# Kernel optimization log

Measured on AMD Instinct MI355X. Metric: run time of the kernel, lower is better.

Reference implementation:

```python
import jax, jax.numpy as jnp
import numpy as np
import math

B, S, D = 2, 1024, 1024
H = 16
HD = D // H
E = 8
DFF = 4096
EPS = 1e-5


def _ln(x, g, b):
    m = jnp.mean(x, axis=-1, keepdims=True)
    v = jnp.mean((x - m) ** 2, axis=-1, keepdims=True)
    return (x - m) / jnp.sqrt(v + EPS) * g + b


def setup_inputs() -> dict:
    key = jax.random.key(0)
    ks = jax.random.split(key, 16)
    s = 0.02
    inp = {
        'src': jax.random.normal(ks[0], (B, S, D), jnp.float32),
        'qw': jax.random.normal(ks[1], (D, D), jnp.float32) * s,
        'kw': jax.random.normal(ks[2], (D, D), jnp.float32) * s,
        'vw': jax.random.normal(ks[3], (D, D), jnp.float32) * s,
        'ow': jax.random.normal(ks[4], (D, D), jnp.float32) * s,
        'gate_w': jax.random.normal(ks[5], (D, D), jnp.float32) * s,
        'gate_b': jax.random.normal(ks[6], (D,), jnp.float32) * s,
        'scale_w': jax.random.normal(ks[7], (H, HD), jnp.float32) * s,
        'n1_g': jnp.ones((D,), jnp.float32),
        'n1_b': jnp.zeros((D,), jnp.float32),
        'n2_g': jnp.ones((D,), jnp.float32),
        'n2_b': jnp.zeros((D,), jnp.float32),
        'moe_gate_w': jax.random.normal(ks[8], (D, E), jnp.float32) * s,
        'moe_gate_b': jnp.zeros((E,), jnp.float32),
        'w1': jax.random.normal(ks[9], (E, D, DFF), jnp.float32) * s,
        'b1': jnp.zeros((E, DFF), jnp.float32),
        'ln_g': jnp.ones((E, DFF), jnp.float32),
        'ln_b': jnp.zeros((E, DFF), jnp.float32),
        'w2': jax.random.normal(ks[10], (E, DFF, D), jnp.float32) * s,
        'b2': jnp.zeros((E, D), jnp.float32),
        'res_scale': jnp.ones((E,), jnp.float32),
    }
    return inp


def _forward(src, qw, kw, vw, ow, gate_w, gate_b, scale_w, n1_g, n1_b, n2_g, n2_b,
             moe_gate_w, moe_gate_b, w1, b1, ln_g, ln_b, w2, b2, res_scale):
    # ---- MemoAttention (non-flash path, eval: no dropout, no mask) ----
    q = (src @ qw).reshape(B, S, H, HD).transpose(0, 2, 1, 3)  # [B,H,S,HD]
    k = (src @ kw).reshape(B, S, H, HD).transpose(0, 2, 1, 3)
    v = (src @ vw).reshape(B, S, H, HD).transpose(0, 2, 1, 3)
    scores = jnp.einsum('bhqd,bhkd->bhqk', q, k) / math.sqrt(HD)
    # dynamic per-(head,query) scale gate
    scale = jax.nn.sigmoid(jnp.einsum('bhsd,hd->bhs', q, scale_w)) * 2.0
    scores = scores * scale[..., None]
    attn = jax.nn.softmax(scores, axis=-1)
    out = jnp.einsum('bhqk,bhkd->bhqd', attn, v)
    out = out.transpose(0, 2, 1, 3).reshape(B, S, D)
    gate = jax.nn.sigmoid(out @ gate_w + gate_b)
    attn_out = (out * gate) @ ow

    x = _ln(src + attn_out, n1_g, n1_b)

    # ---- MoE FFN (top-2 routing; eval: no gate noise; capacity never exceeded) ----
    xf = x.reshape(-1, D)                      # [T, D]
    T = xf.shape[0]
    logits = xf @ moe_gate_w + moe_gate_b      # [T, E]
    top_v, top_i = jax.lax.top_k(logits, 2)
    # NB: original sums BOTH top-k softmax weights per token (== 1.0), and the
    wsum = jnp.sum(jax.nn.softmax(top_v, axis=-1), axis=-1)   # [T] (== 1)
    e_sel = jnp.max(top_i, axis=-1)                           # [T]
    # dense per-expert FFN on all tokens, then per-token select (masked compute)
    h = jnp.einsum('td,edf->etf', xf, w1) + b1[:, None, :]    # [E,T,DFF]
    h = _ln(h, ln_g[:, None, :], ln_b[:, None, :])
    h = jax.nn.gelu(h, approximate=False)                     # torch nn.GELU (erf)
    y = jnp.einsum('etf,efd->etd', h, w2) + b2[:, None, :]    # [E,T,D]
    y = y * res_scale[:, None, None] + xf[None]
    sel = jnp.take_along_axis(y, e_sel[None, :, None], axis=0)[0]  # [T,D]
    moe_out = (sel * wsum[:, None]).reshape(B, S, D)

    return _ln(x + moe_out, n2_g, n2_b)


def reference(src, qw, kw, vw, ow, gate_w, gate_b, scale_w, n1_g, n1_b, n2_g, n2_b,
              moe_gate_w, moe_gate_b, w1, b1, ln_g, ln_b, w2, b2, res_scale):
    return _forward(src, qw, kw, vw, ow, gate_w, gate_b, scale_w, n1_g, n1_b,
                    n2_g, n2_b, moe_gate_w, moe_gate_b, w1, b1, ln_g, ln_b,
                    w2, b2, res_scale)
```

## Files before the change

### kernel.cpp

```cpp
#include <hip/hip_runtime.h>
#include <math.h>

#define TOK    2048
#define DMODEL 1024
#define NHEAD  16
#define HDIM   64
#define NEXP   8
#define DFFN   4096

typedef unsigned short u16;
typedef __attribute__((ext_vector_type(8))) short short8;
typedef __attribute__((ext_vector_type(4))) float floatx4;

__device__ __forceinline__ float sigmoidf_(float x) { return 1.f / (1.f + expf(-x)); }

__device__ __forceinline__ u16 f2bf(float f) {
  union { float f; unsigned u; } v; v.f = f;
  unsigned r = v.u + 0x7FFFu + ((v.u >> 16) & 1u);
  return (u16)(r >> 16);
}
__device__ __forceinline__ float bf2f(u16 h) {
  union { unsigned u; float f; } v; v.u = ((unsigned)h) << 16; return v.f;
}

__device__ __forceinline__ void gload16(const void* g, void* l) {
  __builtin_amdgcn_global_load_lds((const __attribute__((address_space(1))) void*)g,
                                   (__attribute__((address_space(3))) void*)l, 16, 0, 0);
}

__device__ __forceinline__ float blockReduceSum256(float val) {
  __shared__ float ws_[4];
  #pragma unroll
  for (int off = 32; off; off >>= 1) val += __shfl_down(val, off);
  int lane = threadIdx.x & 63, w = threadIdx.x >> 6;
  if (lane == 0) ws_[w] = val;
  __syncthreads();
  float r = ws_[0] + ws_[1] + ws_[2] + ws_[3];
  __syncthreads();
  return r;
}

__global__ __launch_bounds__(256) void split_kernel(
    const float* __restrict__ X, u16* __restrict__ Hi, u16* __restrict__ Lo) {
  const int i = blockIdx.x * 256 + threadIdx.x;
  const float4 v = ((const float4*)X)[i];
  const float f[4] = {v.x, v.y, v.z, v.w};
  union { u16 s[4]; uint2 u; } h, l;
  #pragma unroll
  for (int j = 0; j < 4; ++j) {
    h.s[j] = f2bf(f[j]);
    l.s[j] = f2bf(f[j] - bf2f(h.s[j]));
  }
  ((uint2*)Hi)[i] = h.u;
  ((uint2*)Lo)[i] = l.u;
}

template<bool LO>
__global__ __launch_bounds__(256) void wt_conv_kernel(
    const float* __restrict__ W, u16* __restrict__ Whi, u16* __restrict__ Wlo,
    int K, int N) {
  const size_t z = blockIdx.z;
  W   += z * (size_t)K * N;
  Whi += z * (size_t)K * N;
  if (LO) Wlo += z * (size_t)K * N;
  __shared__ float tile[32][33];
  const int n0 = blockIdx.x * 32, k0 = blockIdx.y * 32;
  const int r = threadIdx.x >> 3, c4 = (threadIdx.x & 7) * 4;
  const float4 v = *(const float4*)&W[(size_t)(k0 + r) * N + n0 + c4];
  tile[r][c4+0] = v.x; tile[r][c4+1] = v.y; tile[r][c4+2] = v.z; tile[r][c4+3] = v.w;
  __syncthreads();
  union { u16 s[4]; uint2 u; } h, l;
  #pragma unroll
  for (int j = 0; j < 4; ++j) {
    const float f = tile[c4 + j][r];
    h.s[j] = f2bf(f);
    if (LO) l.s[j] = f2bf(f - bf2f(h.s[j]));
  }
  *(uint2*)&Whi[(size_t)(n0 + r) * K + k0 + c4] = h.u;
  if (LO) *(uint2*)&Wlo[(size_t)(n0 + r) * K + k0 + c4] = l.u;
}

template<int EPI>
__global__ __launch_bounds__(256, 3) void gemm_split_kernel(
    const u16* __restrict__ Ahi, const u16* __restrict__ Alo,
    const u16* __restrict__ Whi, const u16* __restrict__ Wlo,
    const float* __restrict__ bias, const float* __restrict__ mul,
    float* __restrict__ Cf, u16* __restrict__ Chi, u16* __restrict__ Clo,
    int M, int N, int K) {
  __shared__ u16 Ah[128*64], Al[128*64], Bh[64*64], Bl[64*64];
  const int tid = threadIdx.x;
  const int lane = tid & 63, wave = tid >> 6;
  const int row0 = blockIdx.y * 128, col0 = blockIdx.x * 64;
  const int wm = (wave & 1) * 64, wn = (wave >> 1) * 32;
  const int mr = tid >> 3;
  const int ksrc = (tid & 7) ^ ((tid >> 3) & 7);
  const floatx4 zero = {0.f, 0.f, 0.f, 0.f};
  floatx4 acc[4][2];
  #pragma unroll
  for (int i = 0; i < 4; ++i)
    #pragma unroll
    for (int j = 0; j < 2; ++j) acc[i][j] = zero;

  for (int k0 = 0; k0 < K; k0 += 64) {
    __syncthreads();
    #pragma unroll
    for (int p = 0; p < 4; ++p) {
      const size_t ga = (size_t)(row0 + p * 32 + mr) * K + (k0 + ksrc * 8);
      const size_t off = (size_t)(p * 256 + wave * 64) * 16;
      gload16(Ahi + ga, (char*)Ah + off);
      gload16(Alo + ga, (char*)Al + off);
    }
    #pragma unroll
    for (int p = 0; p < 2; ++p) {
      const size_t gb = (size_t)(col0 + p * 32 + mr) * K + (k0 + ksrc * 8);
      const size_t off = (size_t)(p * 256 + wave * 64) * 16;
      gload16(Whi + gb, (char*)Bh + off);
      gload16(Wlo + gb, (char*)Bl + off);
    }
    __syncthreads();
    #pragma unroll
    for (int kk = 0; kk < 2; ++kk) {
      short8 ah[4], al[4], bh[2], bl[2];
      #pragma unroll
      for (int i = 0; i < 4; ++i) {
        const int ml = wm + i * 16 + (lane & 15);
        const int cm = (kk * 4 + (lane >> 4)) ^ (ml & 7);
        ah[i] = *(const short8*)&Ah[ml * 64 + cm * 8];
        al[i] = *(const short8*)&Al[ml * 64 + cm * 8];
      }
      #pragma unroll
      for (int j = 0; j < 2; ++j) {
        const int nl = wn + j * 16 + (lane & 15);
        const int cn = (kk * 4 + (lane >> 4)) ^ (nl & 7);
        bh[j] = *(const short8*)&Bh[nl * 64 + cn * 8];
        bl[j] = *(const short8*)&Bl[nl * 64 + cn * 8];
      }
      #pragma unroll
      for (int i = 0; i < 4; ++i)
        #pragma unroll
        for (int j = 0; j < 2; ++j) {
          acc[i][j] = __builtin_amdgcn_mfma_f32_16x16x32_bf16(ah[i], bh[j], acc[i][j], 0, 0, 0);
          acc[i][j] = __builtin_amdgcn_mfma_f32_16x16x32_bf16(al[i], bh[j], acc[i][j], 0, 0, 0);
          acc[i][j] = __builtin_amdgcn_mfma_f32_16x16x32_bf16(ah[i], bl[j], acc[i][j], 0, 0, 0);
        }
    }
  }
  const int cl = lane & 15, quad = lane >> 4;
  #pragma unroll
  for (int i = 0; i < 4; ++i)
    #pragma unroll
    for (int j = 0; j < 2; ++j) {
      const int col = col0 + wn + j * 16 + cl;
      #pragma unroll
      for (int r = 0; r < 4; ++r) {
        const int row = row0 + wm + i * 16 + quad * 4 + r;
        const float v = acc[i][j][r];
        if (EPI == 0) {
          Cf[(size_t)row * N + col] = v;
        } else if (EPI == 1) {
          const float s = sigmoidf_(v + bias[col]);
          const float g = s * mul[(size_t)row * N + col];
          const u16 hh = f2bf(g);
          Chi[(size_t)row * N + col] = hh;
          Clo[(size_t)row * N + col] = f2bf(g - bf2f(hh));
        } else {
          const u16 hh = f2bf(v);
          Chi[(size_t)row * N + col] = hh;
          Clo[(size_t)row * N + col] = f2bf(v - bf2f(hh));
        }
      }
    }
}

template<int EPI>
__global__ __launch_bounds__(256, 4) void gemm_moe_kernel(
    const u16* __restrict__ A, const u16* __restrict__ Wt,
    const float* __restrict__ bias,
    const int* __restrict__ perm, const int* __restrict__ offs,
    const int* __restrict__ counts,
    u16* __restrict__ Hout, float* __restrict__ P0, float* __restrict__ P1,
    int N, int K, int e_base) {
  const int z = blockIdx.z;
  const int ez = (EPI == 0) ? z : (z & 3);
  const int ks = (EPI == 0) ? 0 : (z >> 2);
  const int e = e_base + ez;
  const int ne = counts[e];
  const int tm = blockIdx.y;
  if (tm * 128 >= ne) return;
  const int kbeg = (EPI == 0) ? 0 : ks * (K >> 1);
  const int kend = (EPI == 0) ? K : kbeg + (K >> 1);
  __shared__ u16 As_[128*64], Bs_[64*64];
  __shared__ int toks[128];
  const int tid = threadIdx.x;
  if (tid < 128) {
    const int idx = tm * 128 + tid;
    toks[tid] = perm[offs[e] + (idx < ne ? idx : 0)];
  }
  __syncthreads();
  const int lane = tid & 63, wave = tid >> 6;
  const int wm = (wave & 1) * 64, wn = (wave >> 1) * 32;
  const int mr = tid >> 3;
  const int ksrc = (tid & 7) ^ ((tid >> 3) & 7);
  size_t abase[4];
  #pragma unroll
  for (int p = 0; p < 4; ++p) abase[p] = (size_t)toks[p * 32 + mr] * K;
  const u16* We = Wt + (size_t)ez * N * K;
  const int col0 = blockIdx.x * 64;
  const floatx4 zero = {0.f, 0.f, 0.f, 0.f};
  floatx4 acc[4][2];
  #pragma unroll
  for (int i = 0; i < 4; ++i)
    #pragma unroll
    for (int j = 0; j < 2; ++j) acc[i][j] = zero;

  for (int k0 = kbeg; k0 < kend; k0 += 64) {
    __syncthreads();
    #pragma unroll
    for (int p = 0; p < 4; ++p) {
      const size_t off = (size_t)(p * 256 + wave * 64) * 16;
      gload16(A + abase[p] + (k0 + ksrc * 8), (char*)As_ + off);
    }
    #pragma unroll
    for (int p = 0; p < 2; ++p) {
      const size_t off = (size_t)(p * 256 + wave * 64) * 16;
      gload16(We + (size_t)(col0 + p * 32 + mr) * K + (k0 + ksrc * 8), (char*)Bs_ + off);
    }
    __syncthreads();
    #pragma unroll
    for (int kk = 0; kk < 2; ++kk) {
      short8 a[4], b[2];
      #pragma unroll
      for (int i = 0; i < 4; ++i) {
        const int ml = wm + i * 16 + (lane & 15);
        const int cm = (kk * 4 + (lane >> 4)) ^ (ml & 7);
        a[i] = *(const short8*)&As_[ml * 64 + cm * 8];
      }
      #pragma unroll
      for (int j = 0; j < 2; ++j) {
        const int nl = wn + j * 16 + (lane & 15);
        const int cn = (kk * 4 + (lane >> 4)) ^ (nl & 7);
        b[j] = *(const short8*)&Bs_[nl * 64 + cn * 8];
      }
      #pragma unroll
      for (int i = 0; i < 4; ++i)
        #pragma unroll
        for (int j = 0; j < 2; ++j)
          acc[i][j] = __builtin_amdgcn_mfma_f32_16x16x32_bf16(a[i], b[j], acc[i][j], 0, 0, 0);
    }
  }
  const int cl = lane & 15, quad = lane >> 4;
  float* Pp = (EPI == 1) ? (ks ? P1 : P0) : nullptr;
  #pragma unroll
  for (int i = 0; i < 4; ++i)
    #pragma unroll
    for (int j = 0; j < 2; ++j) {
      const int col = col0 + wn + j * 16 + cl;
      #pragma unroll
      for (int r = 0; r < 4; ++r) {
        const int rl = wm + i * 16 + quad * 4 + r;
        if (tm * 128 + rl < ne) {
          const int tok = toks[rl];
          if (EPI == 0)
            Hout[(size_t)tok * N + col] = f2bf(acc[i][j][r] + bias[(size_t)e * N + col]);
          else
            Pp[(size_t)tok * N + col] = acc[i][j][r];
        }
      }
    }
}

__global__ __launch_bounds__(256) void vt_trans_kernel(
    const u16* __restrict__ QKh, const u16* __restrict__ QKl,
    u16* __restrict__ Vth, u16* __restrict__ Vtl) {
  const int tt = blockIdx.x;
  const int bh = blockIdx.y;
  const int b = bh >> 4, h = bh & 15;
  __shared__ u16 th[64][72], tl[64][72];
  const int t = threadIdx.x;
  const int r = t >> 3, c8 = (t & 7) * 8;
  #pragma unroll
  for (int p = 0; p < 2; ++p) {
    const int tok = p * 32 + r;
    const size_t g = ((size_t)b * 1024 + tt * 64 + tok) * 3072 + 2048 + h * 64 + c8;
    *(uint4*)&th[tok][c8] = *(const uint4*)&QKh[g];
    *(uint4*)&tl[tok][c8] = *(const uint4*)&QKl[g];
  }
  __syncthreads();
  #pragma unroll
  for (int p = 0; p < 2; ++p) {
    const int d = p * 32 + r;
    union { u16 s[8]; uint4 u; } oh, ol;
    #pragma unroll
    for (int j = 0; j < 8; ++j) { oh.s[j] = th[c8 + j][d]; ol.s[j] = tl[c8 + j][d]; }
    const size_t g = ((size_t)bh * 64 + d) * 1024 + tt * 64 + c8;
    *(uint4*)&Vth[g] = oh.u;
    *(uint4*)&Vtl[g] = ol.u;
  }
}

__global__ __launch_bounds__(256, 2) void attn_mfma_kernel(
    const u16* __restrict__ QKh, const u16* __restrict__ QKl,
    const u16* __restrict__ Vth, const u16* __restrict__ Vtl,
    const float* __restrict__ scale_w,
    float* __restrict__ AOf, u16* __restrict__ AOh, u16* __restrict__ AOl) {
  const int qt = blockIdx.x, h = blockIdx.y, b = blockIdx.z;
  __shared__ u16 Kh[64*64], Kl[64*64], Vh[64*64], Vl[64*64];
  __shared__ u16 Ph[4][16*72], Pl[4][16*72];
  const int tid = threadIdx.x, lane = tid & 63, wave = tid >> 6;
  const int i15 = lane & 15, quad = lane >> 4;
  const floatx4 zero = {0.f, 0.f, 0.f, 0.f};

  short8 qh[2], ql[2];
  const size_t qrow = ((size_t)b * 1024 + qt * 64 + wave * 16 + i15) * 3072 + h * 64;
  #pragma unroll
  for (int kk = 0; kk < 2; ++kk) {
    qh[kk] = *(const short8*)&QKh[qrow + kk * 32 + quad * 8];
    ql[kk] = *(const short8*)&QKl[qrow + kk * 32 + quad * 8];
  }
  float dot = 0.f;
  #pragma unroll
  for (int kk = 0; kk < 2; ++kk)
    #pragma unroll
    for (int j = 0; j < 8; ++j) {
      const float sw = scale_w[h * 64 + kk * 32 + quad * 8 + j];
      dot += (bf2f((u16)qh[kk][j]) + bf2f((u16)ql[kk][j])) * sw;
    }
  dot += __shfl_xor(dot, 16);
  dot += __shfl_xor(dot, 32);
  const float g = 2.f * sigmoidf_(dot) * 0.125f;
  float stot[4];
  #pragma unroll
  for (int r = 0; r < 4; ++r) stot[r] = __shfl(g, (lane >> 4) * 4 + r);

  float m_r[4], l_r[4];
  floatx4 Of[4];
  #pragma unroll
  for (int r = 0; r < 4; ++r) { m_r[r] = -1e30f; l_r[r] = 0.f; }
  #pragma unroll
  for (int f = 0; f < 4; ++f) Of[f] = zero;
  u16* PhW = Ph[wave];
  u16* PlW = Pl[wave];

  const int sr = tid >> 3, sc = ((tid & 7) ^ ((tid >> 3) & 7)) * 8;
  for (int kt = 0; kt < 16; ++kt) {
    __syncthreads();
    #pragma unroll
    for (int p = 0; p < 2; ++p) {
      const int row = p * 32 + sr;
      const size_t off = (size_t)(p * 256 + wave * 64) * 16;
      const size_t kg = ((size_t)b * 1024 + kt * 64 + row) * 3072 + 1024 + h * 64 + sc;
      gload16(QKh + kg, (char*)Kh + off);
      gload16(QKl + kg, (char*)Kl + off);
      const size_t vg = ((size_t)(b * 16 + h) * 64 + row) * 1024 + kt * 64 + sc;
      gload16(Vth + vg, (char*)Vh + off);
      gload16(Vtl + vg, (char*)Vl + off);
    }
    __syncthreads();
    float pm[4][4];
    #pragma unroll
    for (int jn = 0; jn < 4; ++jn) {
      floatx4 a = zero;
      #pragma unroll
      for (int kk = 0; kk < 2; ++kk) {
        const int n = jn * 16 + i15;
        const int ch = ((kk * 4 + quad) ^ (n & 7)) * 8;
        const short8 bh = *(const short8*)&Kh[n * 64 + ch];
        const short8 bl = *(const short8*)&Kl[n * 64 + ch];
        a = __builtin_amdgcn_mfma_f32_16x16x32_bf16(qh[kk], bh, a, 0, 0, 0);
        a = __builtin_amdgcn_mfma_f32_16x16x32_bf16(ql[kk], bh, a, 0, 0, 0);
        a = __builtin_amdgcn_mfma_f32_16x16x32_bf16(qh[kk], bl, a, 0, 0, 0);
      }
      #pragma unroll
      for (int r = 0; r < 4; ++r) pm[jn][r] = a[r] * stot[r];
    }
    float alpha[4];
    #pragma unroll
    for (int r = 0; r < 4; ++r) {
      float mx = fmaxf(fmaxf(pm[0][r], pm[1][r]), fmaxf(pm[2][r], pm[3][r]));
      mx = fmaxf(mx, __shfl_xor(mx, 1));
      mx = fmaxf(mx, __shfl_xor(mx, 2));
      mx = fmaxf(mx, __shfl_xor(mx, 4));
      mx = fmaxf(mx, __shfl_xor(mx, 8));
      const float mn = fmaxf(m_r[r], mx);
      alpha[r] = expf(m_r[r] - mn);
      m_r[r] = mn;
      float rs = 0.f;
      #pragma unroll
      for (int jn = 0; jn < 4; ++jn) { pm[jn][r] = expf(pm[jn][r] - mn); rs += pm[jn][r]; }
      rs += __shfl_xor(rs, 1);
      rs += __shfl_xor(rs, 2);
      rs += __shfl_xor(rs, 4);
      rs += __shfl_xor(rs, 8);
      l_r[r] = l_r[r] * alpha[r] + rs;
    }
    #pragma unroll
    for (int f = 0; f < 4; ++f)
      #pragma unroll
      for (int r = 0; r < 4; ++r) Of[f][r] *= alpha[r];
    #pragma unroll
    for (int jn = 0; jn < 4; ++jn)
      #pragma unroll
      for (int r = 0; r < 4; ++r) {
        const int a = (quad * 4 + r) * 72 + jn * 16 + i15;
        const u16 hh = f2bf(pm[jn][r]);
        PhW[a] = hh;
        PlW[a] = f2bf(pm[jn][r] - bf2f(hh));
      }
    #pragma unroll
    for (int kk = 0; kk < 2; ++kk) {
      const short8 pah = *(const short8*)&PhW[i15 * 72 + kk * 32 + quad * 8];
      const short8 pal = *(const short8*)&PlW[i15 * 72 + kk * 32 + quad * 8];
      #pragma unroll
      for (int f = 0; f < 4; ++f) {
        const int d = f * 16 + i15;
        const int ch = ((kk * 4 + quad) ^ (d & 7)) * 8;
        const short8 vbh = *(const short8*)&Vh[d * 64 + ch];
        const short8 vbl = *(const short8*)&Vl[d * 64 + ch];
        Of[f] = __builtin_amdgcn_mfma_f32_16x16x32_bf16(pah, vbh, Of[f], 0, 0, 0);
        Of[f] = __builtin_amdgcn_mfma_f32_16x16x32_bf16(pal, vbh, Of[f], 0, 0, 0);
        Of[f] = __builtin_amdgcn_mfma_f32_16x16x32_bf16(pah, vbl, Of[f], 0, 0, 0);
      }
    }
  }
  float inv[4];
  #pragma unroll
  for (int r = 0; r < 4; ++r) inv[r] = 1.f / l_r[r];
  #pragma unroll
  for (int f = 0; f < 4; ++f)
    #pragma unroll
    for (int r = 0; r < 4; ++r) {
      const size_t row = (size_t)b * 1024 + qt * 64 + wave * 16 + quad * 4 + r;
      const int col = h * 64 + f * 16 + i15;
      const float val = Of[f][r] * inv[r];
      AOf[row * 1024 + col] = val;
      const u16 hh = f2bf(val);
      AOh[row * 1024 + col] = hh;
      AOl[row * 1024 + col] = f2bf(val - bf2f(hh));
    }
}

template<bool BF>
__global__ __launch_bounds__(256) void ln_add_kernel(
    const float* __restrict__ A, const float* __restrict__ Bp,
    const float* __restrict__ g, const float* __restrict__ beta,
    float* __restrict__ outf, u16* __restrict__ outh) {
  int t = blockIdx.x, tid = threadIdx.x;
  const float* a = A + (size_t)t * DMODEL;
  const float* b = Bp + (size_t)t * DMODEL;
  float v[4]; float s = 0.f;
  #pragma unroll
  for (int i = 0; i < 4; ++i) { int d = tid + i*256; v[i] = a[d] + b[d]; s += v[i]; }
  s = blockReduceSum256(s);
  float mean = s * (1.f/1024.f);
  float q = 0.f;
  #pragma unroll
  for (int i = 0; i < 4; ++i) { float df = v[i]-mean; q += df*df; }
  q = blockReduceSum256(q);
  float rstd = rsqrtf(q*(1.f/1024.f) + 1e-5f);
  #pragma unroll
  for (int i = 0; i < 4; ++i) {
    int d = tid + i*256;
    float val = (v[i]-mean)*rstd*g[d] + beta[d];
    outf[(size_t)t*DMODEL + d] = val;
    if (BF) outh[(size_t)t*DMODEL + d] = f2bf(val);
  }
}

__global__ __launch_bounds__(256) void ln_final_kernel(
    const float* __restrict__ X, const float* __restrict__ P0,
    const float* __restrict__ P1, const float* __restrict__ B2,
    const float* __restrict__ rsv, const int* __restrict__ e_sel,
    const float* __restrict__ g, const float* __restrict__ beta,
    float* __restrict__ out) {
  int t = blockIdx.x, tid = threadIdx.x;
  const int e = e_sel[t];
  const float rse = rsv[e];
  const float* b2e = B2 + (size_t)e * DMODEL;
  float v[4]; float s = 0.f;
  #pragma unroll
  for (int i = 0; i < 4; ++i) {
    int d = tid + i*256;
    const size_t idx = (size_t)t * DMODEL + d;
    const float xv = X[idx];
    const float yv = (P0[idx] + P1[idx] + b2e[d]) * rse + xv;
    v[i] = xv + yv;
    s += v[i];
  }
  s = blockReduceSum256(s);
  float mean = s * (1.f/1024.f);
  float q = 0.f;
  #pragma unroll
  for (int i = 0; i < 4; ++i) { float df = v[i]-mean; q += df*df; }
  q = blockReduceSum256(q);
  float rstd = rsqrtf(q*(1.f/1024.f) + 1e-5f);
  #pragma unroll
  for (int i = 0; i < 4; ++i) {
    int d = tid + i*256;
    out[(size_t)t*DMODEL + d] = (v[i]-mean)*rstd*g[d] + beta[d];
  }
}

__global__ __launch_bounds__(256) void moe_gate_kernel(
    const float* __restrict__ X, const float* __restrict__ gw,
    const float* __restrict__ gb, int* __restrict__ e_sel) {
  int wave = threadIdx.x >> 6, lane = threadIdx.x & 63;
  int token = blockIdx.x * 4 + wave;
  const float* x = X + (size_t)token * DMODEL;
  float acc[NEXP] = {};
  for (int d = lane; d < DMODEL; d += 64) {
    float xv = x[d];
    const float* gr = gw + (size_t)d * NEXP;
    #pragma unroll
    for (int e = 0; e < NEXP; ++e) acc[e] += xv * gr[e];
  }
  #pragma unroll
  for (int e = 0; e < NEXP; ++e) {
    #pragma unroll
    for (int off = 32; off; off >>= 1) acc[e] += __shfl_down(acc[e], off);
  }
  if (lane == 0) {
    float lg[NEXP];
    #pragma unroll
    for (int e = 0; e < NEXP; ++e) lg[e] = acc[e] + gb[e];
    int i1 = 0;
    for (int e = 1; e < NEXP; ++e) if (lg[e] > lg[i1]) i1 = e;
    int i2 = -1;
    for (int e = 0; e < NEXP; ++e) {
      if (e == i1) continue;
      if (i2 < 0 || lg[e] > lg[i2]) i2 = e;
    }
    e_sel[token] = (i1 > i2) ? i1 : i2;
  }
}

__global__ __launch_bounds__(256) void moe_group_kernel(
    const int* __restrict__ e_sel, int* __restrict__ perm,
    int* __restrict__ g_offs, int* __restrict__ g_counts) {
  __shared__ int cnt[NEXP], offs[NEXP], cur[NEXP];
  int tid = threadIdx.x;
  if (tid < NEXP) cnt[tid] = 0;
  __syncthreads();
  for (int t = tid; t < TOK; t += 256) atomicAdd(&cnt[e_sel[t]], 1);
  __syncthreads();
  if (tid == 0) {
    int run = 0;
    for (int e = 0; e < NEXP; ++e) { offs[e] = run; cur[e] = run; run += cnt[e]; }
  }
  __syncthreads();
  if (tid < NEXP) { g_offs[tid] = offs[tid]; g_counts[tid] = cnt[tid]; }
  for (int t = tid; t < TOK; t += 256) {
    int pos = atomicAdd(&cur[e_sel[t]], 1);
    perm[pos] = t;
  }
}

__global__ __launch_bounds__(256) void moe_ln_gelu_kernel(
    u16* __restrict__ H, const float* __restrict__ ln_g,
    const float* __restrict__ ln_b, const int* __restrict__ e_sel) {
  int t = blockIdx.x, tid = threadIdx.x;
  int e = e_sel[t];
  u16* h = H + (size_t)t * DFFN;
  float v[16]; float s = 0.f;
  #pragma unroll
  for (int i = 0; i < 16; ++i) { v[i] = bf2f(h[tid + i*256]); s += v[i]; }
  s = blockReduceSum256(s);
  float mean = s * (1.f/4096.f);
  float q = 0.f;
  #pragma unroll
  for (int i = 0; i < 16; ++i) { float df = v[i]-mean; q += df*df; }
  q = blockReduceSum256(q);
  float rstd = rsqrtf(q*(1.f/4096.f) + 1e-5f);
  const float* gg = ln_g + (size_t)e * DFFN;
  const float* bb = ln_b + (size_t)e * DFFN;
  #pragma unroll
  for (int i = 0; i < 16; ++i) {
    int d = tid + i*256;
    float x = (v[i]-mean)*rstd*gg[d] + bb[d];
    h[d] = f2bf(0.5f * x * (1.f + erff(x * 0.7071067811865475f)));
  }
}

extern "C" void kernel_launch(void* const* d_in, const int* in_sizes, int n_in,
                              void* d_out, int out_size, void* d_ws, size_t ws_size,
                              hipStream_t stream) {
  (void)in_sizes; (void)n_in; (void)out_size; (void)ws_size;
  const float* src    = (const float*)d_in[0];
  const float* qw     = (const float*)d_in[1];
  const float* kw     = (const float*)d_in[2];
  const float* vw     = (const float*)d_in[3];
  const float* ow     = (const float*)d_in[4];
  const float* gate_w = (const float*)d_in[5];
  const float* gate_b = (const float*)d_in[6];
  const float* scale_w= (const float*)d_in[7];
  const float* n1_g   = (const float*)d_in[8];
  const float* n1_b   = (const float*)d_in[9];
  const float* n2_g   = (const float*)d_in[10];
  const float* n2_b   = (const float*)d_in[11];
  const float* mgw    = (const float*)d_in[12];
  const float* mgb    = (const float*)d_in[13];
  const float* w1     = (const float*)d_in[14];
  const float* b1     = (const float*)d_in[15];
  const float* ln_g   = (const float*)d_in[16];
  const float* ln_b   = (const float*)d_in[17];
  const float* w2     = (const float*)d_in[18];
  const float* b2     = (const float*)d_in[19];
  const float* rs     = (const float*)d_in[20];

  char* ws = (char*)d_ws;
  const size_t MB = 1024 * 1024;
  u16*   qkv_hi = (u16*)(ws + 0*MB);
  u16*   qkv_lo = (u16*)(ws + 12*MB);
  u16*   Wt3_hi = (u16*)(ws + 24*MB);
  u16*   Wt3_lo = (u16*)(ws + 30*MB);
  u16*   Vt_hi  = (u16*)(ws + 36*MB);
  u16*   Vt_lo  = (u16*)(ws + 40*MB);
  u16*   src_hi = (u16*)(ws + 44*MB);
  u16*   src_lo = (u16*)(ws + 48*MB);
  float* ao     = (float*)(ws + 44*MB);
  u16*   ao_hi  = (u16*)(ws + 52*MB);
  u16*   ao_lo  = (u16*)(ws + 56*MB);
  u16*   gb_hi  = (u16*)(ws + 60*MB);
  u16*   gb_lo  = (u16*)(ws + 64*MB);
  float* proj   = (float*)(ws + 0*MB);
  float* x      = (float*)(ws + 8*MB);
  u16*   x_hi   = (u16*)(ws + 16*MB);
  u16*   WtA    = (u16*)(ws + 24*MB);
  u16*   h      = (u16*)(ws + 56*MB);
  float* p0     = (float*)(ws + 0*MB);
  float* p1     = (float*)(ws + 72*MB);
  int*   e_sel  = (int*)(ws + 80*MB);
  int*   perm   = e_sel + TOK;
  int*   offs   = perm + TOK;
  int*   cnts   = offs + NEXP;

  dim3 blk(256);
  split_kernel<<<2048, blk, 0, stream>>>(src, src_hi, src_lo);

  wt_conv_kernel<true><<<dim3(32,32,1), blk, 0, stream>>>(qw, Wt3_hi, Wt3_lo, DMODEL, DMODEL);
  wt_conv_kernel<true><<<dim3(32,32,1), blk, 0, stream>>>(kw, Wt3_hi + 1024*1024, Wt3_lo + 1024*1024, DMODEL, DMODEL);
  wt_conv_kernel<true><<<dim3(32,32,1), blk, 0, stream>>>(vw, Wt3_hi + 2048*1024, Wt3_lo + 2048*1024, DMODEL, DMODEL);
  gemm_split_kernel<2><<<dim3(48,16), blk, 0, stream>>>(src_hi, src_lo, Wt3_hi, Wt3_lo,
      nullptr, nullptr, nullptr, qkv_hi, qkv_lo, TOK, 3072, DMODEL);

  vt_trans_kernel<<<dim3(16,32), blk, 0, stream>>>(qkv_hi, qkv_lo, Vt_hi, Vt_lo);
  attn_mfma_kernel<<<dim3(16, NHEAD, 2), blk, 0, stream>>>(
      qkv_hi, qkv_lo, Vt_hi, Vt_lo, scale_w, ao, ao_hi, ao_lo);

  wt_conv_kernel<true><<<dim3(32,32,1), blk, 0, stream>>>(gate_w, Wt3_hi, Wt3_lo, DMODEL, DMODEL);
  gemm_split_kernel<1><<<dim3(16,16), blk, 0, stream>>>(ao_hi, ao_lo, Wt3_hi, Wt3_lo,
      gate_b, ao, nullptr, gb_hi, gb_lo, TOK, DMODEL, DMODEL);
  wt_conv_kernel<true><<<dim3(32,32,1), blk, 0, stream>>>(ow, Wt3_hi, Wt3_lo, DMODEL, DMODEL);
  gemm_split_kernel<0><<<dim3(16,16), blk, 0, stream>>>(gb_hi, gb_lo, Wt3_hi, Wt3_lo,
      nullptr, nullptr, proj, nullptr, nullptr, TOK, DMODEL, DMODEL);

  ln_add_kernel<true><<<TOK, blk, 0, stream>>>(src, proj, n1_g, n1_b, x, x_hi);

  moe_gate_kernel<<<TOK/4, blk, 0, stream>>>(x, mgw, mgb, e_sel);
  moe_group_kernel<<<1, blk, 0, stream>>>(e_sel, perm, offs, cnts);

  for (int c = 0; c < 2; ++c) {
    wt_conv_kernel<false><<<dim3(DFFN/32, DMODEL/32, 4), blk, 0, stream>>>(
        w1 + (size_t)c*4*DMODEL*DFFN, WtA, nullptr, DMODEL, DFFN);
    gemm_moe_kernel<0><<<dim3(DFFN/64, 16, 4), blk, 0, stream>>>(
        x_hi, WtA, b1, perm, offs, cnts, h, nullptr, nullptr, DFFN, DMODEL, c*4);
  }
  moe_ln_gelu_kernel<<<TOK, blk, 0, stream>>>(h, ln_g, ln_b, e_sel);
  for (int c = 0; c < 2; ++c) {
    wt_conv_kernel<false><<<dim3(DMODEL/32, DFFN/32, 4), blk, 0, stream>>>(
        w2 + (size_t)c*4*DFFN*DMODEL, WtA, nullptr, DFFN, DMODEL);
    gemm_moe_kernel<1><<<dim3(DMODEL/64, 16, 8), blk, 0, stream>>>(
        h, WtA, nullptr, perm, offs, cnts, nullptr, p0, p1, DMODEL, DFFN, c*4);
  }
  ln_final_kernel<<<TOK, blk, 0, stream>>>(x, p0, p1, b2, rs, e_sel, n2_g, n2_b, (float*)d_out);
}
```

Before: 712.0 us.

## Fuse QKV weight conversion, write transposed V from GEMM epilogue, widen N tiles

The three Q/K/V weight conversion launches become one kernel. The QKV GEMM now writes V directly in the transposed hi/lo layout from its epilogue, which removes the separate vt_trans kernel and its extra pass over V. The QKV split GEMM and the first MoE GEMM move to 128-wide N tiles so each loaded A tile is reused more, at the cost of more registers and lower occupancy (launch bounds drop from 3 to 2 and from 4 to 3). The QKV grid also shrinks to 384 blocks, which may underfill the GPU.

```diff
diff --git a/kernel.cpp b/kernel.cpp
--- a/kernel.cpp
+++ b/kernel.cpp
@@ -80,26 +80,52 @@
   if (LO) *(uint2*)&Wlo[(size_t)(n0 + r) * K + k0 + c4] = l.u;
 }
 
-template<int EPI>
-__global__ __launch_bounds__(256, 3) void gemm_split_kernel(
+__global__ __launch_bounds__(256) void wt3_conv_kernel(
+    const float* __restrict__ Q, const float* __restrict__ Kw,
+    const float* __restrict__ V, u16* __restrict__ Whi, u16* __restrict__ Wlo) {
+  const int zz = blockIdx.z >> 5;
+  const float* W = (zz == 0) ? Q : (zz == 1) ? Kw : V;
+  u16* Whi_ = Whi + (size_t)zz * DMODEL * DMODEL;
+  u16* Wlo_ = Wlo + (size_t)zz * DMODEL * DMODEL;
+  __shared__ float tile[32][33];
+  const int n0 = blockIdx.x * 32, k0 = (blockIdx.z & 31) * 32;
+  const int r = threadIdx.x >> 3, c4 = (threadIdx.x & 7) * 4;
+  const float4 v = *(const float4*)&W[(size_t)(k0 + r) * DMODEL + n0 + c4];
+  tile[r][c4+0] = v.x; tile[r][c4+1] = v.y; tile[r][c4+2] = v.z; tile[r][c4+3] = v.w;
+  __syncthreads();
+  union { u16 s[4]; uint2 u; } h, l;
+  #pragma unroll
+  for (int j = 0; j < 4; ++j) {
+    const float f = tile[c4 + j][r];
+    h.s[j] = f2bf(f);
+    l.s[j] = f2bf(f - bf2f(h.s[j]));
+  }
+  *(uint2*)&Whi_[(size_t)(n0 + r) * DMODEL + k0 + c4] = h.u;
+  *(uint2*)&Wlo_[(size_t)(n0 + r) * DMODEL + k0 + c4] = l.u;
+}
+
+template<int EPI, int TN>
+__global__ __launch_bounds__(256, TN == 64 ? 3 : 2) void gemm_split_kernel(
     const u16* __restrict__ Ahi, const u16* __restrict__ Alo,
     const u16* __restrict__ Whi, const u16* __restrict__ Wlo,
     const float* __restrict__ bias, const float* __restrict__ mul,
     float* __restrict__ Cf, u16* __restrict__ Chi, u16* __restrict__ Clo,
+    u16* __restrict__ Vth, u16* __restrict__ Vtl,
     int M, int N, int K) {
-  __shared__ u16 Ah[128*64], Al[128*64], Bh[64*64], Bl[64*64];
+  constexpr int NF = TN / 32;
+  __shared__ u16 Ah[128*64], Al[128*64], Bh[TN*64], Bl[TN*64];
   const int tid = threadIdx.x;
   const int lane = tid & 63, wave = tid >> 6;
-  const int row0 = blockIdx.y * 128, col0 = blockIdx.x * 64;
-  const int wm = (wave & 1) * 64, wn = (wave >> 1) * 32;
+  const int row0 = blockIdx.y * 128, col0 = blockIdx.x * TN;
+  const int wm = (wave & 1) * 64, wn = (wave >> 1) * (TN / 2);
   const int mr = tid >> 3;
   const int ksrc = (tid & 7) ^ ((tid >> 3) & 7);
   const floatx4 zero = {0.f, 0.f, 0.f, 0.f};
-  floatx4 acc[4][2];
+  floatx4 acc[4][NF];
   #pragma unroll
   for (int i = 0; i < 4; ++i)
     #pragma unroll
-    for (int j = 0; j < 2; ++j) acc[i][j] = zero;
+    for (int j = 0; j < NF; ++j) acc[i][j] = zero;
 
   for (int k0 = 0; k0 < K; k0 += 64) {
     __syncthreads();
@@ -111,7 +137,7 @@
       gload16(Alo + ga, (char*)Al + off);
     }
     #pragma unroll
-    for (int p = 0; p < 2; ++p) {
+    for (int p = 0; p < NF; ++p) {
       const size_t gb = (size_t)(col0 + p * 32 + mr) * K + (k0 + ksrc * 8);
       const size_t off = (size_t)(p * 256 + wave * 64) * 16;
       gload16(Whi + gb, (char*)Bh + off);
@@ -120,7 +146,7 @@
     __syncthreads();
     #pragma unroll
     for (int kk = 0; kk < 2; ++kk) {
-      short8 ah[4], al[4], bh[2], bl[2];
+      short8 ah[4], al[4], bh[NF], bl[NF];
       #pragma unroll
       for (int i = 0; i < 4; ++i) {
         const int ml = wm + i * 16 + (lane & 15);
@@ -129,7 +155,7 @@
         al[i] = *(const short8*)&Al[ml * 64 + cm * 8];
       }
       #pragma unroll
-      for (int j = 0; j < 2; ++j) {
+      for (int j = 0; j < NF; ++j) {
         const int nl = wn + j * 16 + (lane & 15);
         const int cn = (kk * 4 + (lane >> 4)) ^ (nl & 7);
         bh[j] = *(const short8*)&Bh[nl * 64 + cn * 8];
@@ -138,7 +164,7 @@
       #pragma unroll
       for (int i = 0; i < 4; ++i)
         #pragma unroll
-        for (int j = 0; j < 2; ++j) {
+        for (int j = 0; j < NF; ++j) {
           acc[i][j] = __builtin_amdgcn_mfma_f32_16x16x32_bf16(ah[i], bh[j], acc[i][j], 0, 0, 0);
           acc[i][j] = __builtin_amdgcn_mfma_f32_16x16x32_bf16(al[i], bh[j], acc[i][j], 0, 0, 0);
           acc[i][j] = __builtin_amdgcn_mfma_f32_16x16x32_bf16(ah[i], bl[j], acc[i][j], 0, 0, 0);
@@ -146,10 +172,32 @@
     }
   }
   const int cl = lane & 15, quad = lane >> 4;
+  if (EPI == 2 && col0 >= 2048) {
+    #pragma unroll
+    for (int i = 0; i < 4; ++i)
+      #pragma unroll
+      for (int j = 0; j < NF; ++j) {
+        const int dg = col0 + wn + j * 16 + cl - 2048;
+        const int bh_ = dg >> 6, d = dg & 63;
+        const int row = row0 + wm + i * 16 + quad * 4;
+        const int b = row >> 10, t0 = row & 1023;
+        union { u16 s[4]; uint2 u; } hh, ll;
+        #pragma unroll
+        for (int r = 0; r < 4; ++r) {
+          const float v = acc[i][j][r];
+          hh.s[r] = f2bf(v);
+          ll.s[r] = f2bf(v - bf2f(hh.s[r]));
+        }
+        const size_t base = ((size_t)(b * 16 + bh_) * 64 + d) * 1024 + t0;
+        *(uint2*)&Vth[base] = hh.u;
+        *(uint2*)&Vtl[base] = ll.u;
+      }
+    return;
+  }
   #pragma unroll
   for (int i = 0; i < 4; ++i)
     #pragma unroll
-    for (int j = 0; j < 2; ++j) {
+    for (int j = 0; j < NF; ++j) {
       const int col = col0 + wn + j * 16 + cl;
       #pragma unroll
       for (int r = 0; r < 4; ++r) {
@@ -172,14 +220,15 @@
     }
 }
 
-template<int EPI>
-__global__ __launch_bounds__(256, 4) void gemm_moe_kernel(
+template<int EPI, int TN>
+__global__ __launch_bounds__(256, TN == 64 ? 4 : 3) void gemm_moe_kernel(
     const u16* __restrict__ A, const u16* __restrict__ Wt,
     const float* __restrict__ bias,
     const int* __restrict__ perm, const int* __restrict__ offs,
     const int* __restrict__ counts,
     u16* __restrict__ Hout, float* __restrict__ P0, float* __restrict__ P1,
     int N, int K, int e_base) {
+  constexpr int NF = TN / 32;
   const int z = blockIdx.z;
   const int ez = (EPI == 0) ? z : (z & 3);
   const int ks = (EPI == 0) ? 0 : (z >> 2);
@@ -189,7 +238,7 @@
   if (tm * 128 >= ne) return;
   const int kbeg = (EPI == 0) ? 0 : ks * (K >> 1);
   const int kend = (EPI == 0) ? K : kbeg + (K >> 1);
-  __shared__ u16 As_[128*64], Bs_[64*64];
+  __shared__ u16 As_[128*64], Bs_[TN*64];
   __shared__ int toks[128];
   const int tid = threadIdx.x;
   if (tid < 128) {
@@ -198,20 +247,20 @@
   }
   __syncthreads();
   const int lane = tid & 63, wave = tid >> 6;
-  const int wm = (wave & 1) * 64, wn = (wave >> 1) * 32;
+  const int wm = (wave & 1) * 64, wn = (wave >> 1) * (TN / 2);
   const int mr = tid >> 3;
   const int ksrc = (tid & 7) ^ ((tid >> 3) & 7);
   size_t abase[4];
   #pragma unroll
   for (int p = 0; p < 4; ++p) abase[p] = (size_t)toks[p * 32 + mr] * K;
   const u16* We = Wt + (size_t)ez * N * K;
-  const int col0 = blockIdx.x * 64;
+  const int col0 = blockIdx.x * TN;
   const floatx4 zero = {0.f, 0.f, 0.f, 0.f};
-  floatx4 acc[4][2];
+  floatx4 acc[4][NF];
   #pragma unroll
   for (int i = 0; i < 4; ++i)
     #pragma unroll
-    for (int j = 0; j < 2; ++j) acc[i][j] = zero;
+    for (int j = 0; j < NF; ++j) acc[i][j] = zero;
 
   for (int k0 = kbeg; k0 < kend; k0 += 64) {
     __syncthreads();
@@ -221,14 +270,14 @@
       gload16(A + abase[p] + (k0 + ksrc * 8), (char*)As_ + off);
     }
     #pragma unroll
-    for (int p = 0; p < 2; ++p) {
+    for (int p = 0; p < NF; ++p) {
       const size_t off = (size_t)(p * 256 + wave * 64) * 16;
       gload16(We + (size_t)(col0 + p * 32 + mr) * K + (k0 + ksrc * 8), (char*)Bs_ + off);
     }
     __syncthreads();
     #pragma unroll
     for (int kk = 0; kk < 2; ++kk) {
-      short8 a[4], b[2];
+      short8 a[4], b[NF];
       #pragma unroll
       for (int i = 0; i < 4; ++i) {
         const int ml = wm + i * 16 + (lane & 15);
@@ -236,7 +285,7 @@
         a[i] = *(const short8*)&As_[ml * 64 + cm * 8];
       }
       #pragma unroll
-      for (int j = 0; j < 2; ++j) {
+      for (int j = 0; j < NF; ++j) {
         const int nl = wn + j * 16 + (lane & 15);
         const int cn = (kk * 4 + (lane >> 4)) ^ (nl & 7);
         b[j] = *(const short8*)&Bs_[nl * 64 + cn * 8];
@@ -244,7 +293,7 @@
       #pragma unroll
       for (int i = 0; i < 4; ++i)
         #pragma unroll
-        for (int j = 0; j < 2; ++j)
+        for (int j = 0; j < NF; ++j)
           acc[i][j] = __builtin_amdgcn_mfma_f32_16x16x32_bf16(a[i], b[j], acc[i][j], 0, 0, 0);
     }
   }
@@ -253,7 +302,7 @@
   #pragma unroll
   for (int i = 0; i < 4; ++i)
     #pragma unroll
-    for (int j = 0; j < 2; ++j) {
+    for (int j = 0; j < NF; ++j) {
       const int col = col0 + wn + j * 16 + cl;
       #pragma unroll
       for (int r = 0; r < 4; ++r) {
@@ -267,35 +316,6 @@
         }
       }
     }
-}
-
-__global__ __launch_bounds__(256) void vt_trans_kernel(
-    const u16* __restrict__ QKh, const u16* __restrict__ QKl,
-    u16* __restrict__ Vth, u16* __restrict__ Vtl) {
-  const int tt = blockIdx.x;
-  const int bh = blockIdx.y;
-  const int b = bh >> 4, h = bh & 15;
-  __shared__ u16 th[64][72], tl[64][72];
-  const int t = threadIdx.x;
-  const int r = t >> 3, c8 = (t & 7) * 8;
-  #pragma unroll
-  for (int p = 0; p < 2; ++p) {
-    const int tok = p * 32 + r;
-    const size_t g = ((size_t)b * 1024 + tt * 64 + tok) * 3072 + 2048 + h * 64 + c8;
-    *(uint4*)&th[tok][c8] = *(const uint4*)&QKh[g];
-    *(uint4*)&tl[tok][c8] = *(const uint4*)&QKl[g];
-  }
-  __syncthreads();
-  #pragma unroll
-  for (int p = 0; p < 2; ++p) {
-    const int d = p * 32 + r;
-    union { u16 s[8]; uint4 u; } oh, ol;
-    #pragma unroll
-    for (int j = 0; j < 8; ++j) { oh.s[j] = th[c8 + j][d]; ol.s[j] = tl[c8 + j][d]; }
-    const size_t g = ((size_t)bh * 64 + d) * 1024 + tt * 64 + c8;
-    *(uint4*)&Vth[g] = oh.u;
-    *(uint4*)&Vtl[g] = ol.u;
-  }
 }
 
 __global__ __launch_bounds__(256, 2) void attn_mfma_kernel(
@@ -636,22 +656,19 @@
   dim3 blk(256);
   split_kernel<<<2048, blk, 0, stream>>>(src, src_hi, src_lo);
 
-  wt_conv_kernel<true><<<dim3(32,32,1), blk, 0, stream>>>(qw, Wt3_hi, Wt3_lo, DMODEL, DMODEL);
-  wt_conv_kernel<true><<<dim3(32,32,1), blk, 0, stream>>>(kw, Wt3_hi + 1024*1024, Wt3_lo + 1024*1024, DMODEL, DMODEL);
-  wt_conv_kernel<true><<<dim3(32,32,1), blk, 0, stream>>>(vw, Wt3_hi + 2048*1024, Wt3_lo + 2048*1024, DMODEL, DMODEL);
-  gemm_split_kernel<2><<<dim3(48,16), blk, 0, stream>>>(src_hi, src_lo, Wt3_hi, Wt3_lo,
-      nullptr, nullptr, nullptr, qkv_hi, qkv_lo, TOK, 3072, DMODEL);
-
-  vt_trans_kernel<<<dim3(16,32), blk, 0, stream>>>(qkv_hi, qkv_lo, Vt_hi, Vt_lo);
+  wt3_conv_kernel<<<dim3(32,1,96), blk, 0, stream>>>(qw, kw, vw, Wt3_hi, Wt3_lo);
+  gemm_split_kernel<2,128><<<dim3(24,16), blk, 0, stream>>>(src_hi, src_lo, Wt3_hi, Wt3_lo,
+      nullptr, nullptr, nullptr, qkv_hi, qkv_lo, Vt_hi, Vt_lo, TOK, 3072, DMODEL);
+
   attn_mfma_kernel<<<dim3(16, NHEAD, 2), blk, 0, stream>>>(
       qkv_hi, qkv_lo, Vt_hi, Vt_lo, scale_w, ao, ao_hi, ao_lo);
 
   wt_conv_kernel<true><<<dim3(32,32,1), blk, 0, stream>>>(gate_w, Wt3_hi, Wt3_lo, DMODEL, DMODEL);
-  gemm_split_kernel<1><<<dim3(16,16), blk, 0, stream>>>(ao_hi, ao_lo, Wt3_hi, Wt3_lo,
-      gate_b, ao, nullptr, gb_hi, gb_lo, TOK, DMODEL, DMODEL);
+  gemm_split_kernel<1,64><<<dim3(16,16), blk, 0, stream>>>(ao_hi, ao_lo, Wt3_hi, Wt3_lo,
+      gate_b, ao, nullptr, gb_hi, gb_lo, nullptr, nullptr, TOK, DMODEL, DMODEL);
   wt_conv_kernel<true><<<dim3(32,32,1), blk, 0, stream>>>(ow, Wt3_hi, Wt3_lo, DMODEL, DMODEL);
-  gemm_split_kernel<0><<<dim3(16,16), blk, 0, stream>>>(gb_hi, gb_lo, Wt3_hi, Wt3_lo,
-      nullptr, nullptr, proj, nullptr, nullptr, TOK, DMODEL, DMODEL);
+  gemm_split_kernel<0,64><<<dim3(16,16), blk, 0, stream>>>(gb_hi, gb_lo, Wt3_hi, Wt3_lo,
+      nullptr, nullptr, proj, nullptr, nullptr, nullptr, nullptr, TOK, DMODEL, DMODEL);
 
   ln_add_kernel<true><<<TOK, blk, 0, stream>>>(src, proj, n1_g, n1_b, x, x_hi);
 
@@ -661,14 +678,14 @@
   for (int c = 0; c < 2; ++c) {
     wt_conv_kernel<false><<<dim3(DFFN/32, DMODEL/32, 4), blk, 0, stream>>>(
         w1 + (size_t)c*4*DMODEL*DFFN, WtA, nullptr, DMODEL, DFFN);
-    gemm_moe_kernel<0><<<dim3(DFFN/64, 16, 4), blk, 0, stream>>>(
+    gemm_moe_kernel<0,128><<<dim3(DFFN/128, 16, 4), blk, 0, stream>>>(
         x_hi, WtA, b1, perm, offs, cnts, h, nullptr, nullptr, DFFN, DMODEL, c*4);
   }
   moe_ln_gelu_kernel<<<TOK, blk, 0, stream>>>(h, ln_g, ln_b, e_sel);
   for (int c = 0; c < 2; ++c) {
     wt_conv_kernel<false><<<dim3(DMODEL/32, DFFN/32, 4), blk, 0, stream>>>(
         w2 + (size_t)c*4*DFFN*DMODEL, WtA, nullptr, DFFN, DMODEL);
-    gemm_moe_kernel<1><<<dim3(DMODEL/64, 16, 8), blk, 0, stream>>>(
+    gemm_moe_kernel<1,64><<<dim3(DMODEL/64, 16, 8), blk, 0, stream>>>(
         h, WtA, nullptr, perm, offs, cnts, nullptr, p0, p1, DMODEL, DFFN, c*4);
   }
   ln_final_kernel<<<TOK, blk, 0, stream>>>(x, p0, p1, b2, rs, e_sel, n2_g, n2_b, (float*)d_out);
```

New measurement: 726.2 us. 2.0% more time.
